# Optimization experiments

Hardware: AMD Instinct MI355X
Metric: run time of the kernel (lower is better)

## Reference

```python
import jax, jax.numpy as jnp
import numpy as np

N, E, B = 100000, 3200000, 1024
D_LM, K, H, C, L = 1024, 128, 256, 40, 2
T = 0.1
LN_EPS = 1e-5


def _layernorm(x, g, b):
    m = x.mean(-1, keepdims=True)
    v = ((x - m) ** 2).mean(-1, keepdims=True)
    return (x - m) * jax.lax.rsqrt(v + LN_EPS) * g + b


def _gcn_conv(x, W, b, src, dst, norm, self_w):
    h = x @ W
    agg = jax.ops.segment_sum(h[src] * norm[:, None], dst, num_segments=N)
    return agg + h * self_w[:, None] + b


def setup_inputs() -> dict:
    key = jax.random.key(0)
    ks = jax.random.split(key, 20)
    s = 0.02
    rn = lambda k, shp: jax.random.normal(k, shp, jnp.float32) * s
    return {
        "hidden_embeds": jax.random.normal(ks[0], (L, N, D_LM), jnp.float32),
        "proj_W1": rn(ks[1], (L, D_LM, K)),
        "proj_b1": jnp.zeros((L, K), jnp.float32),
        "ln_g": jnp.ones((L, K), jnp.float32),
        "ln_b": jnp.zeros((L, K), jnp.float32),
        "proj_W2": rn(ks[2], (L, K, K)),
        "proj_b2": jnp.zeros((L, K), jnp.float32),
        "alphas": jnp.zeros((L,), jnp.float32),
        "gcn_W1": rn(ks[3], (L, K, H)),
        "gcn_b1": jnp.zeros((L, H), jnp.float32),
        "gcn_W2": rn(ks[4], (L, H, K)),
        "gcn_b2": jnp.zeros((L, K), jnp.float32),
        "clf_W": rn(ks[5], (2 * K, C)),
        "clf_b": jnp.zeros((C,), jnp.float32),
        "edge_index": jax.random.randint(ks[6], (2, E), 0, N, jnp.int64 if jax.config.jax_enable_x64 else jnp.int32),
        "mapping": jax.random.randint(ks[7], (B,), 0, N, jnp.int64 if jax.config.jax_enable_x64 else jnp.int32),
    }


def reference(hidden_embeds, proj_W1, proj_b1, ln_g, ln_b, proj_W2, proj_b2,
              alphas, gcn_W1, gcn_b1, gcn_W2, gcn_b2, clf_W, clf_b,
              edge_index, mapping):
    src, dst = edge_index[0], edge_index[1]
    ones = jnp.ones((E,), jnp.float32)
    # GCN normalization (self loops included): deg over dst + 1
    deg = jax.ops.segment_sum(ones, dst, num_segments=N) + 1.0
    dis = jax.lax.rsqrt(deg)
    norm = dis[src] * dis[dst]          # per-edge D^-1/2 A D^-1/2
    self_w = 1.0 / deg                  # self-loop weight dis[i]*dis[i]

    last = None
    for i in range(L):
        # projector: Linear -> LayerNorm -> ReLU -> Linear
        h = hidden_embeds[i] @ proj_W1[i] + proj_b1[i]
        h = jax.nn.relu(_layernorm(h, ln_g[i], ln_b[i]))
        h = h @ proj_W2[i] + proj_b2[i]
        if i > 0:
            a = jax.nn.sigmoid(alphas[i] / T)
            h = h * a + last * (1.0 - a)
        # 2-layer GCN encoder (dropout=0)
        z = jax.nn.relu(_gcn_conv(h, gcn_W1[i], gcn_b1[i], src, dst, norm, self_w))
        last = _gcn_conv(z, gcn_W2[i], gcn_b2[i], src, dst, norm, self_w)

    # custom_global_mean_pool: mean over {node} U {out-neighbors} U {in-neighbors}
    sum_n = (jax.ops.segment_sum(last[dst], src, num_segments=N)
             + jax.ops.segment_sum(last[src], dst, num_segments=N))
    cnt = (jax.ops.segment_sum(ones, src, num_segments=N)
           + jax.ops.segment_sum(ones, dst, num_segments=N))
    pooled = (last[mapping] + sum_n[mapping]) / (1.0 + cnt[mapping])[:, None]

    out = jnp.concatenate([last[mapping], pooled], axis=1)  # [B, 2K]
    return out @ clf_W + clf_b
```

## Files before the change

### kernel.cpp

```cpp
#include <hip/hip_runtime.h>
#include <hip/hip_bf16.h>
#include <math.h>

using short8 = __attribute__((ext_vector_type(8))) short;
using f32x4  = __attribute__((ext_vector_type(4))) float;

#define PSTRIDE 2048

__device__ __forceinline__ short f2bf(float f) {
    __hip_bfloat16 h = __float2bfloat16(f);
    return *reinterpret_cast<short*>(&h);
}


__global__ void map_scatter_k(const int* __restrict__ mapping, int* __restrict__ map_idx, int B)
{
    int b = blockIdx.x * blockDim.x + threadIdx.x;
    if (b < B) map_idx[mapping[b]] = b;
}

__launch_bounds__(1024)
__global__ void bin_count_k(const int* __restrict__ dst, int E, int* __restrict__ bin_cnt)
{
    __shared__ int h[4096];
    for (int i = threadIdx.x; i < 4096; i += 1024) h[i] = 0;
    __syncthreads();
    int base = blockIdx.x * 32768;
#pragma unroll
    for (int i = 0; i < 32; ++i) {
        int e = base + i * 1024 + threadIdx.x;
        if (e < E) atomicAdd(&h[dst[e] >> 5], 1);
    }
    __syncthreads();
    for (int i = threadIdx.x; i < 4096; i += 1024) {
        int c = h[i];
        if (c) atomicAdd(&bin_cnt[i], c);
    }
}

__launch_bounds__(1024)
__global__ void scan_bins_k(const int* __restrict__ cnt, int* __restrict__ off,
                            int* __restrict__ cur)
{
    __shared__ int wsum[16];
    int tid = threadIdx.x, lane = tid & 63, wid = tid >> 6;
    int4 v = ((const int4*)cnt)[tid];
    int s0 = v.x, s1 = s0 + v.y, s2 = s1 + v.z, s3 = s2 + v.w;
    int q = s3;
#pragma unroll
    for (int o = 1; o < 64; o <<= 1) { int t = __shfl_up(q, o); if (lane >= o) q += t; }
    if (lane == 63) wsum[wid] = q;
    __syncthreads();
    if (wid == 0) {
        int w = (lane < 16) ? wsum[lane] : 0;
#pragma unroll
        for (int o = 1; o < 16; o <<= 1) { int t = __shfl_up(w, o); if (lane >= o) w += t; }
        if (lane < 16) wsum[lane] = w;
    }
    __syncthreads();
    int base = (wid ? wsum[wid - 1] : 0) + q - s3;
    int4 o4; o4.x = base; o4.y = base + s0; o4.z = base + s1; o4.w = base + s2;
    ((int4*)off)[tid] = o4;
    ((int4*)cur)[tid] = o4;
    if (tid == 1023) off[4096] = base + s3;
}

__launch_bounds__(256)
__global__ void bin_scatter_k(const int* __restrict__ ei, int E,
                              const int* __restrict__ map_idx,
                              int* __restrict__ bin_cur, int2* __restrict__ pairs,
                              int* __restrict__ pcnt, int* __restrict__ pnb)
{
    int e = blockIdx.x * blockDim.x + threadIdx.x;
    if (e >= E) return;
    int s = ei[e];
    int d = ei[E + e];
    int p = atomicAdd(&bin_cur[d >> 5], 1);
    pairs[p] = make_int2(s, d);
    int ms = map_idx[s];
    if (ms >= 0) {
        int i = atomicAdd(&pcnt[ms], 1);
        if (i < PSTRIDE) pnb[ms * PSTRIDE + i] = d;
    }
    int md = map_idx[d];
    if (md >= 0) {
        int i = atomicAdd(&pcnt[md], 1);
        if (i < PSTRIDE) pnb[md * PSTRIDE + i] = s;
    }
}

__launch_bounds__(256)
__global__ void bin_csr_k(const int2* __restrict__ pairs, const int* __restrict__ bin_off,
                          int* __restrict__ csr_in, int* __restrict__ in_off,
                          float* __restrict__ dis, float* __restrict__ selfw, int N)
{
    __shared__ int lcnt[32];
    __shared__ int lofs[32];
    __shared__ int lcur[32];
    int b = blockIdx.x;
    int tid = threadIdx.x;
    if (tid < 32) lcnt[tid] = 0;
    __syncthreads();
    int beg = bin_off[b], end = bin_off[b + 1];
    for (int i = beg + tid; i < end; i += 256)
        atomicAdd(&lcnt[pairs[i].y & 31], 1);
    __syncthreads();
    if (tid == 0) {
        int run = beg;
#pragma unroll
        for (int j = 0; j < 32; ++j) { lofs[j] = run; lcur[j] = run; run += lcnt[j]; }
    }
    __syncthreads();
    int n0 = b * 32;
    if (tid < 32 && n0 + tid < N) {
        in_off[n0 + tid] = lofs[tid];
        float dg = (float)lcnt[tid] + 1.0f;
        dis[n0 + tid] = rsqrtf(dg);
        selfw[n0 + tid] = 1.0f / dg;
    }
    if (b == gridDim.x - 1 && tid == 0) in_off[N] = end;
    for (int i = beg + tid; i < end; i += 256) {
        int2 pr = pairs[i];
        int p = atomicAdd(&lcur[pr.y & 31], 1);
        csr_in[p] = pr.x;
    }
}

__global__ void transpose_w_k(const float* __restrict__ src, short* __restrict__ dst,
                              int R, int Cc)
{
    int idx = blockIdx.x * blockDim.x + threadIdx.x;
    if (idx >= R * Cc) return;
    int r = idx / Cc;
    int c = idx - r * Cc;
    dst[(size_t)c * R + r] = f2bf(src[idx]);
}

__launch_bounds__(256)
__global__ void proj_fused_k(const float* __restrict__ X,
                             const short* __restrict__ W1t,
                             const float* __restrict__ b1,
                             const float* __restrict__ lng,
                             const float* __restrict__ lnb,
                             const short* __restrict__ W2t,
                             const float* __restrict__ b2,
                             const float* __restrict__ alphas, int layer,
                             const float* __restrict__ last,
                             short* __restrict__ out, int nrows)
{
    __shared__ short S[26112];

    const int tid  = threadIdx.x;
    const int lane = tid & 63;
    const int wave = tid >> 6;
    const int g    = lane >> 4;
    const int lr   = lane & 15;
    const int wrow = wave * 16;
    const int row0 = blockIdx.x * 64;

    f32x4 acc[8];
#pragma unroll
    for (int f = 0; f < 8; ++f) acc[f] = (f32x4){0.f, 0.f, 0.f, 0.f};

    for (int k0 = 0; k0 < 1024; k0 += 64) {
        {
            int r  = tid >> 2;
            int c0 = (tid & 3) * 16;
            int gr = row0 + r;
            float4 v0 = make_float4(0.f,0.f,0.f,0.f), v1 = v0, v2 = v0, v3 = v0;
            if (gr < nrows) {
                const float* xp = X + (size_t)gr * 1024 + k0 + c0;
                v0 = *(const float4*)&xp[0];
                v1 = *(const float4*)&xp[4];
                v2 = *(const float4*)&xp[8];
                v3 = *(const float4*)&xp[12];
            }
            short8 p0, p1;
            p0[0]=f2bf(v0.x); p0[1]=f2bf(v0.y); p0[2]=f2bf(v0.z); p0[3]=f2bf(v0.w);
            p0[4]=f2bf(v1.x); p0[5]=f2bf(v1.y); p0[6]=f2bf(v1.z); p0[7]=f2bf(v1.w);
            p1[0]=f2bf(v2.x); p1[1]=f2bf(v2.y); p1[2]=f2bf(v2.z); p1[3]=f2bf(v2.w);
            p1[4]=f2bf(v3.x); p1[5]=f2bf(v3.y); p1[6]=f2bf(v3.z); p1[7]=f2bf(v3.w);
            *(short8*)&S[r * 72 + c0]     = p0;
            *(short8*)&S[r * 72 + c0 + 8] = p1;
        }
        {
            int c  = tid >> 1;
            int kb = (tid & 1) * 32;
            const short* wp = W1t + (size_t)c * 1024 + k0 + kb;
            short* dp = &S[4608 + c * 72 + kb];
#pragma unroll
            for (int m = 0; m < 4; ++m)
                *(short8*)&dp[m * 8] = *(const short8*)&wp[m * 8];
        }
        __syncthreads();
#pragma unroll
        for (int kk = 0; kk < 64; kk += 32) {
            short8 a = *(short8*)&S[(wrow + lr) * 72 + kk + g * 8];
#pragma unroll
            for (int f = 0; f < 8; ++f) {
                short8 b = *(short8*)&S[4608 + (f * 16 + lr) * 72 + kk + g * 8];
                acc[f] = __builtin_amdgcn_mfma_f32_16x16x32_bf16(a, b, acc[f], 0, 0, 0);
            }
        }
        __syncthreads();
    }

    {
        float b1v[8], gv[8], bv[8];
#pragma unroll
        for (int f = 0; f < 8; ++f) {
            int col = f * 16 + lr;
            b1v[f] = b1[col]; gv[f] = lng[col]; bv[f] = lnb[col];
        }
#pragma unroll
        for (int j = 0; j < 4; ++j) {
            float hv[8];
            float s = 0.f, q = 0.f;
#pragma unroll
            for (int f = 0; f < 8; ++f) {
                float t = acc[f][j] + b1v[f];
                hv[f] = t;
                s += t; q += t * t;
            }
#pragma unroll
            for (int m = 1; m < 16; m <<= 1) {
                s += __shfl_xor(s, m);
                q += __shfl_xor(q, m);
            }
            float mean = s * (1.0f / 128.0f);
            float var  = q * (1.0f / 128.0f) - mean * mean;
            float inv  = rsqrtf(var + 1e-5f);
            int rloc = wrow + 4 * g + j;
#pragma unroll
            for (int f = 0; f < 8; ++f) {
                float h = fmaxf((hv[f] - mean) * inv * gv[f] + bv[f], 0.f);
                S[17408 + rloc * 136 + f * 16 + lr] = f2bf(h);
            }
        }
    }
    {
        int c  = tid >> 1;
        int kb = (tid & 1) * 64;
        const short* wp = W2t + (size_t)c * 128 + kb;
        short* dp = &S[c * 136 + kb];
#pragma unroll
        for (int m = 0; m < 8; ++m)
            *(short8*)&dp[m * 8] = *(const short8*)&wp[m * 8];
    }
    __syncthreads();

    f32x4 acc2[8];
#pragma unroll
    for (int f = 0; f < 8; ++f) acc2[f] = (f32x4){0.f, 0.f, 0.f, 0.f};
#pragma unroll
    for (int kk = 0; kk < 128; kk += 32) {
        short8 a = *(short8*)&S[17408 + (wrow + lr) * 136 + kk + g * 8];
#pragma unroll
        for (int f = 0; f < 8; ++f) {
            short8 b = *(short8*)&S[(f * 16 + lr) * 136 + kk + g * 8];
            acc2[f] = __builtin_amdgcn_mfma_f32_16x16x32_bf16(a, b, acc2[f], 0, 0, 0);
        }
    }

    float b2v[8];
#pragma unroll
    for (int f = 0; f < 8; ++f) b2v[f] = b2[f * 16 + lr];
    float asig = 0.f, omas = 0.f;
    if (last) {
        float al = alphas[layer];
        asig = 1.0f / (1.0f + expf(-al * 10.0f));
        omas = 1.0f - asig;
    }
#pragma unroll
    for (int j = 0; j < 4; ++j) {
        int gr = row0 + wrow + 4 * g + j;
        if (gr >= nrows) continue;
#pragma unroll
        for (int f = 0; f < 8; ++f) {
            int col = f * 16 + lr;
            float o = acc2[f][j] + b2v[f];
            if (last) o = asig * o + omas * last[(size_t)gr * 128 + col];
            out[(size_t)gr * 128 + col] = f2bf(o);
        }
    }
}

__launch_bounds__(256)
__global__ void gcn_mlp_k(const short* __restrict__ U,
                          const short* __restrict__ W1t,
                          const float* __restrict__ gb1,
                          const short* __restrict__ W2t,
                          short* __restrict__ V, int M)
{
    __shared__ short S[35840];

    const int tid  = threadIdx.x;
    const int lane = tid & 63;
    const int wave = tid >> 6;
    const int g    = lane >> 4;
    const int lr   = lane & 15;
    const int wrow = wave * 16;
    const int m0   = blockIdx.x * 64;

#pragma unroll
    for (int it = 0; it < 4; ++it) {
        int i = tid + it * 256;
        int r = i >> 4;
        int c8 = i & 15;
        short8 v = {0,0,0,0,0,0,0,0};
        int gr = m0 + r;
        if (gr < M) v = *(const short8*)&U[(size_t)gr * 128 + c8 * 8];
        *(short8*)&S[r * 136 + c8 * 8] = v;
    }

    f32x4 acc[16];
#pragma unroll
    for (int f = 0; f < 16; ++f) acc[f] = (f32x4){0.f, 0.f, 0.f, 0.f};

    for (int k0 = 0; k0 < 128; k0 += 64) {
#pragma unroll
        for (int it = 0; it < 8; ++it) {
            int i = tid + it * 256;
            int r = i >> 3;
            int c8 = i & 7;
            *(short8*)&S[17408 + r * 72 + c8 * 8] =
                *(const short8*)&W1t[(size_t)r * 128 + k0 + c8 * 8];
        }
        __syncthreads();
#pragma unroll
        for (int kk = 0; kk < 64; kk += 32) {
            short8 a = *(short8*)&S[(wrow + lr) * 136 + k0 + kk + g * 8];
#pragma unroll
            for (int f = 0; f < 16; ++f) {
                short8 b = *(short8*)&S[17408 + (f * 16 + lr) * 72 + kk + g * 8];
                acc[f] = __builtin_amdgcn_mfma_f32_16x16x32_bf16(a, b, acc[f], 0, 0, 0);
            }
        }
        __syncthreads();
    }

    {
        float bb[16];
#pragma unroll
        for (int f = 0; f < 16; ++f) bb[f] = gb1[f * 16 + lr];
#pragma unroll
        for (int j = 0; j < 4; ++j) {
            int rloc = wrow + 4 * g + j;
#pragma unroll
            for (int f = 0; f < 16; ++f) {
                float zv = fmaxf(acc[f][j] + bb[f], 0.f);
                S[rloc * 264 + f * 16 + lr] = f2bf(zv);
            }
        }
    }

    f32x4 acc2[8];
#pragma unroll
    for (int f = 0; f < 8; ++f) acc2[f] = (f32x4){0.f, 0.f, 0.f, 0.f};

    for (int k0 = 0; k0 < 256; k0 += 64) {
#pragma unroll
        for (int it = 0; it < 4; ++it) {
            int i = tid + it * 256;
            int r = i >> 3;
            int c8 = i & 7;
            *(short8*)&S[16896 + r * 72 + c8 * 8] =
                *(const short8*)&W2t[(size_t)r * 256 + k0 + c8 * 8];
        }
        __syncthreads();
#pragma unroll
        for (int kk = 0; kk < 64; kk += 32) {
            short8 a = *(short8*)&S[(wrow + lr) * 264 + k0 + kk + g * 8];
#pragma unroll
            for (int f = 0; f < 8; ++f) {
                short8 b = *(short8*)&S[16896 + (f * 16 + lr) * 72 + kk + g * 8];
                acc2[f] = __builtin_amdgcn_mfma_f32_16x16x32_bf16(a, b, acc2[f], 0, 0, 0);
            }
        }
        __syncthreads();
    }

#pragma unroll
    for (int j = 0; j < 4; ++j) {
        int gr = m0 + wrow + 4 * g + j;
        if (gr >= M) continue;
#pragma unroll
        for (int f = 0; f < 8; ++f)
            V[(size_t)gr * 128 + f * 16 + lr] = f2bf(acc2[f][j]);
    }
}

template <bool OUT_BF16>
__launch_bounds__(256)
__global__ void agg_k(const unsigned* __restrict__ x, void* __restrict__ y,
                      const int* __restrict__ off, const int* __restrict__ csr,
                      const float* __restrict__ dis, const float* __restrict__ selfw,
                      const float* __restrict__ bias, int N)
{
    int node = blockIdx.x * 4 + (threadIdx.x >> 6);
    if (node >= N) return;
    int lane = threadIdx.x & 63;
    int beg = off[node], end = off[node + 1];

    float ax0 = 0.f, ay0 = 0.f, ax1 = 0.f, ay1 = 0.f;
    float ax2 = 0.f, ay2 = 0.f, ax3 = 0.f, ay3 = 0.f;
    int e = beg;
    for (; e + 4 <= end; e += 4) {
        int s0 = csr[e], s1 = csr[e + 1], s2 = csr[e + 2], s3 = csr[e + 3];
        unsigned v0 = x[(size_t)s0 * 64 + lane];
        unsigned v1 = x[(size_t)s1 * 64 + lane];
        unsigned v2 = x[(size_t)s2 * 64 + lane];
        unsigned v3 = x[(size_t)s3 * 64 + lane];
        float w0 = dis[s0], w1 = dis[s1], w2 = dis[s2], w3 = dis[s3];
        ax0 = fmaf(w0, __uint_as_float(v0 << 16), ax0);
        ay0 = fmaf(w0, __uint_as_float(v0 & 0xFFFF0000u), ay0);
        ax1 = fmaf(w1, __uint_as_float(v1 << 16), ax1);
        ay1 = fmaf(w1, __uint_as_float(v1 & 0xFFFF0000u), ay1);
        ax2 = fmaf(w2, __uint_as_float(v2 << 16), ax2);
        ay2 = fmaf(w2, __uint_as_float(v2 & 0xFFFF0000u), ay2);
        ax3 = fmaf(w3, __uint_as_float(v3 << 16), ax3);
        ay3 = fmaf(w3, __uint_as_float(v3 & 0xFFFF0000u), ay3);
    }
    for (; e < end; ++e) {
        int s = csr[e];
        float w = dis[s];
        unsigned v = x[(size_t)s * 64 + lane];
        ax0 = fmaf(w, __uint_as_float(v << 16), ax0);
        ay0 = fmaf(w, __uint_as_float(v & 0xFFFF0000u), ay0);
    }
    float accx = (ax0 + ax1) + (ax2 + ax3);
    float accy = (ay0 + ay1) + (ay2 + ay3);

    float dn = dis[node], sw = selfw[node];
    unsigned vo = x[(size_t)node * 64 + lane];
    float rx = dn * accx + sw * __uint_as_float(vo << 16);
    float ry = dn * accy + sw * __uint_as_float(vo & 0xFFFF0000u);
    if (bias) { rx += bias[lane * 2]; ry += bias[lane * 2 + 1]; }
    if (OUT_BF16) {
        unsigned p = (unsigned)(unsigned short)f2bf(rx) | ((unsigned)(unsigned short)f2bf(ry) << 16);
        ((unsigned*)y)[(size_t)node * 64 + lane] = p;
    } else {
        *(float2*)&((float*)y)[(size_t)node * 128 + lane * 2] = make_float2(rx, ry);
    }
}

__launch_bounds__(128)
__global__ void pool_clf_k(const float* __restrict__ last, const int* __restrict__ mapping,
                           const int* __restrict__ map_idx,
                           const int* __restrict__ pcnt, const int* __restrict__ pnb,
                           const float* __restrict__ clfW, const float* __restrict__ clfb,
                           float* __restrict__ out, int C)
{
    int b = blockIdx.x;
    int tid = threadIdx.x;
    int n = mapping[b];
    int rep = map_idx[n];
    int cnt = pcnt[rep];
    int m = cnt < PSTRIDE ? cnt : PSTRIDE;

    float s = 0.f;
    const int* nb = pnb + (size_t)rep * PSTRIDE;
    for (int i = 0; i < m; ++i)
        s += last[(size_t)nb[i] * 128 + tid];

    float lv = last[(size_t)n * 128 + tid];
    float pooled = (lv + s) / (1.0f + (float)cnt);

    __shared__ float feat[256];
    feat[tid] = lv;
    feat[128 + tid] = pooled;
    __syncthreads();

    for (int c = tid; c < C; c += blockDim.x) {
        float o = clfb[c];
        for (int j = 0; j < 256; ++j) o = fmaf(feat[j], clfW[j * C + c], o);
        out[(size_t)b * C + c] = o;
    }
}

extern "C" void kernel_launch(void* const* d_in, const int* in_sizes, int n_in,
                              void* d_out, int out_size, void* d_ws, size_t ws_size,
                              hipStream_t stream)
{
    const float* hidden = (const float*)d_in[0];
    const float* pW1    = (const float*)d_in[1];
    const float* pb1    = (const float*)d_in[2];
    const float* lng    = (const float*)d_in[3];
    const float* lnb    = (const float*)d_in[4];
    const float* pW2    = (const float*)d_in[5];
    const float* pb2    = (const float*)d_in[6];
    const float* alphas = (const float*)d_in[7];
    const float* gW1    = (const float*)d_in[8];
    const float* gb1    = (const float*)d_in[9];
    const float* gW2    = (const float*)d_in[10];
    const float* gb2    = (const float*)d_in[11];
    const float* clfW   = (const float*)d_in[12];
    const float* clfb   = (const float*)d_in[13];
    const int*   ei     = (const int*)d_in[14];
    const int*   mapping= (const int*)d_in[15];

    const int L   = in_sizes[7];
    const int K   = in_sizes[2] / L;
    const int H   = in_sizes[9] / L;
    const int C   = in_sizes[13];
    const int DLM = in_sizes[1] / (L * K);
    const int N   = in_sizes[0] / (L * DLM);
    const int E   = in_sizes[14] / 2;
    const int B   = in_sizes[15];
    const int NBINS = (N + 31) / 32;

    char* ws = (char*)d_ws;
    size_t off = 0;
    auto carve = [&](size_t bytes) -> char* {
        char* p = ws + off;
        off += (bytes + 255) & ~(size_t)255;
        return p;
    };
    int*   map_idx = (int*)carve((size_t)N * 4);
    int*   pcnt    = (int*)carve((size_t)B * 4);
    int*   pnb     = (int*)carve((size_t)B * PSTRIDE * 4);
    int*   bin_cnt = (int*)carve(4096 * 4);
    int*   bin_off = (int*)carve(4097 * 4);
    int*   bin_cur = (int*)carve(4096 * 4);
    int2*  pairs   = (int2*)carve((size_t)E * 8);
    int*   in_off  = (int*)carve((size_t)(N + 1) * 4);
    float* dis     = (float*)carve((size_t)N * 4);
    float* selfw   = (float*)carve((size_t)N * 4);
    int*   csr_in  = (int*)carve((size_t)E * 4);
    short* bufA    = (short*)carve((size_t)N * K * 2);
    short* bufU    = (short*)carve((size_t)N * K * 2);
    float* bufLast = (float*)carve((size_t)N * K * 4);
    short* w1t     = (short*)carve((size_t)L * K * DLM * 2);
    short* w2t     = (short*)carve((size_t)L * K * K * 2);
    short* gw1t    = (short*)carve((size_t)L * H * K * 2);
    short* gw2t    = (short*)carve((size_t)L * K * H * 2);
    (void)ws_size; (void)n_in; (void)out_size;

    hipMemsetAsync(bin_cnt, 0, 4096 * 4, stream);
    hipMemsetAsync(map_idx, 0xFF, (size_t)N * 4, stream);
    hipMemsetAsync(pcnt, 0, (size_t)B * 4, stream);
    map_scatter_k<<<dim3((B + 255) / 256), 256, 0, stream>>>(mapping, map_idx, B);
    bin_count_k<<<dim3((E + 32767) / 32768), 1024, 0, stream>>>(ei + E, E, bin_cnt);
    scan_bins_k<<<dim3(1), 1024, 0, stream>>>(bin_cnt, bin_off, bin_cur);
    bin_scatter_k<<<dim3((E + 255) / 256), 256, 0, stream>>>(ei, E, map_idx, bin_cur,
                                                             pairs, pcnt, pnb);
    bin_csr_k<<<dim3(NBINS), 256, 0, stream>>>(pairs, bin_off, csr_in, in_off,
                                               dis, selfw, N);

    for (int i = 0; i < L; ++i) {
        transpose_w_k<<<dim3((DLM * K + 255) / 256), 256, 0, stream>>>(
            pW1 + (size_t)i * DLM * K, w1t + (size_t)i * K * DLM, DLM, K);
        transpose_w_k<<<dim3((K * K + 255) / 256), 256, 0, stream>>>(
            pW2 + (size_t)i * K * K, w2t + (size_t)i * K * K, K, K);
        transpose_w_k<<<dim3((K * H + 255) / 256), 256, 0, stream>>>(
            gW1 + (size_t)i * K * H, gw1t + (size_t)i * H * K, K, H);
        transpose_w_k<<<dim3((H * K + 255) / 256), 256, 0, stream>>>(
            gW2 + (size_t)i * H * K, gw2t + (size_t)i * K * H, H, K);
    }

    const int nblk64 = (N + 63) / 64;

    for (int i = 0; i < L; ++i) {
        proj_fused_k<<<dim3(nblk64), 256, 0, stream>>>(
            hidden + (size_t)i * N * DLM,
            w1t + (size_t)i * K * DLM,
            pb1 + (size_t)i * K,
            lng + (size_t)i * K,
            lnb + (size_t)i * K,
            w2t + (size_t)i * K * K,
            pb2 + (size_t)i * K,
            alphas, i,
            (i > 0) ? bufLast : nullptr,
            bufA, N);

        agg_k<true><<<dim3((N + 3) / 4), 256, 0, stream>>>(
            (const unsigned*)bufA, bufU, in_off, csr_in, dis, selfw, nullptr, N);
        gcn_mlp_k<<<dim3(nblk64), 256, 0, stream>>>(
            bufU, gw1t + (size_t)i * H * K, gb1 + (size_t)i * H,
            gw2t + (size_t)i * K * H, bufA, N);
        agg_k<false><<<dim3((N + 3) / 4), 256, 0, stream>>>(
            (const unsigned*)bufA, bufLast, in_off, csr_in, dis, selfw,
            gb2 + (size_t)i * K, N);
    }

    pool_clf_k<<<dim3(B), 128, 0, stream>>>(bufLast, mapping, map_idx, pcnt, pnb,
                                            clfW, clfb, (float*)d_out, C);
}
```

Measured before the change: 1.285 ms.

## Double projector tile to 128 rows with 512 threads; unroll edge gather to 8

The fused projector kernel now processes 128 rows per block with 8 waves, so each W1 and W2 tile staged in shared memory is reused by twice as many rows. The W2 stage is reorganised into two 64-wide K chunks so it fits the new LDS layout. Separately, the aggregation kernel unrolls its neighbor gather from 4 to 8 independent loads to raise memory-level parallelism. The costs are fewer blocks in flight and more registers per thread in the aggregation loop.

```diff
diff --git a/kernel.cpp b/kernel.cpp
--- a/kernel.cpp
+++ b/kernel.cpp
@@ -136,7 +136,7 @@
     dst[(size_t)c * R + r] = f2bf(src[idx]);
 }
 
-__launch_bounds__(256)
+__launch_bounds__(512)
 __global__ void proj_fused_k(const float* __restrict__ X,
                              const short* __restrict__ W1t,
                              const float* __restrict__ b1,
@@ -148,7 +148,7 @@
                              const float* __restrict__ last,
                              short* __restrict__ out, int nrows)
 {
-    __shared__ short S[26112];
+    __shared__ short S[26624];
 
     const int tid  = threadIdx.x;
     const int lane = tid & 63;
@@ -156,7 +156,7 @@
     const int g    = lane >> 4;
     const int lr   = lane & 15;
     const int wrow = wave * 16;
-    const int row0 = blockIdx.x * 64;
+    const int row0 = blockIdx.x * 128;
 
     f32x4 acc[8];
 #pragma unroll
@@ -184,13 +184,11 @@
             *(short8*)&S[r * 72 + c0 + 8] = p1;
         }
         {
-            int c  = tid >> 1;
-            int kb = (tid & 1) * 32;
+            int c  = tid >> 2;
+            int kb = (tid & 3) * 16;
             const short* wp = W1t + (size_t)c * 1024 + k0 + kb;
-            short* dp = &S[4608 + c * 72 + kb];
-#pragma unroll
-            for (int m = 0; m < 4; ++m)
-                *(short8*)&dp[m * 8] = *(const short8*)&wp[m * 8];
+            *(short8*)&S[9216 + c * 72 + kb]     = *(const short8*)&wp[0];
+            *(short8*)&S[9216 + c * 72 + kb + 8] = *(const short8*)&wp[8];
         }
         __syncthreads();
 #pragma unroll
@@ -198,7 +196,7 @@
             short8 a = *(short8*)&S[(wrow + lr) * 72 + kk + g * 8];
 #pragma unroll
             for (int f = 0; f < 8; ++f) {
-                short8 b = *(short8*)&S[4608 + (f * 16 + lr) * 72 + kk + g * 8];
+                short8 b = *(short8*)&S[9216 + (f * 16 + lr) * 72 + kk + g * 8];
                 acc[f] = __builtin_amdgcn_mfma_f32_16x16x32_bf16(a, b, acc[f], 0, 0, 0);
             }
         }
@@ -234,32 +232,33 @@
 #pragma unroll
             for (int f = 0; f < 8; ++f) {
                 float h = fmaxf((hv[f] - mean) * inv * gv[f] + bv[f], 0.f);
-                S[17408 + rloc * 136 + f * 16 + lr] = f2bf(h);
-            }
-        }
-    }
-    {
-        int c  = tid >> 1;
-        int kb = (tid & 1) * 64;
-        const short* wp = W2t + (size_t)c * 128 + kb;
-        short* dp = &S[c * 136 + kb];
-#pragma unroll
-        for (int m = 0; m < 8; ++m)
-            *(short8*)&dp[m * 8] = *(const short8*)&wp[m * 8];
-    }
-    __syncthreads();
+                S[rloc * 136 + f * 16 + lr] = f2bf(h);
+            }
+        }
+    }
 
     f32x4 acc2[8];
 #pragma unroll
     for (int f = 0; f < 8; ++f) acc2[f] = (f32x4){0.f, 0.f, 0.f, 0.f};
-#pragma unroll
-    for (int kk = 0; kk < 128; kk += 32) {
-        short8 a = *(short8*)&S[17408 + (wrow + lr) * 136 + kk + g * 8];
-#pragma unroll
-        for (int f = 0; f < 8; ++f) {
-            short8 b = *(short8*)&S[(f * 16 + lr) * 136 + kk + g * 8];
-            acc2[f] = __builtin_amdgcn_mfma_f32_16x16x32_bf16(a, b, acc2[f], 0, 0, 0);
-        }
+    for (int k0 = 0; k0 < 128; k0 += 64) {
+        {
+            int c  = tid >> 2;
+            int kb = (tid & 3) * 16;
+            const short* wp = W2t + (size_t)c * 128 + k0 + kb;
+            *(short8*)&S[17408 + c * 72 + kb]     = *(const short8*)&wp[0];
+            *(short8*)&S[17408 + c * 72 + kb + 8] = *(const short8*)&wp[8];
+        }
+        __syncthreads();
+#pragma unroll
+        for (int kk = 0; kk < 64; kk += 32) {
+            short8 a = *(short8*)&S[(wrow + lr) * 136 + k0 + kk + g * 8];
+#pragma unroll
+            for (int f = 0; f < 8; ++f) {
+                short8 b = *(short8*)&S[17408 + (f * 16 + lr) * 72 + kk + g * 8];
+                acc2[f] = __builtin_amdgcn_mfma_f32_16x16x32_bf16(a, b, acc2[f], 0, 0, 0);
+            }
+        }
+        __syncthreads();
     }
 
     float b2v[8];
@@ -402,34 +401,36 @@
     int lane = threadIdx.x & 63;
     int beg = off[node], end = off[node + 1];
 
-    float ax0 = 0.f, ay0 = 0.f, ax1 = 0.f, ay1 = 0.f;
-    float ax2 = 0.f, ay2 = 0.f, ax3 = 0.f, ay3 = 0.f;
+    float ax[8], ay[8];
+#pragma unroll
+    for (int u = 0; u < 8; ++u) { ax[u] = 0.f; ay[u] = 0.f; }
+
     int e = beg;
-    for (; e + 4 <= end; e += 4) {
-        int s0 = csr[e], s1 = csr[e + 1], s2 = csr[e + 2], s3 = csr[e + 3];
-        unsigned v0 = x[(size_t)s0 * 64 + lane];
-        unsigned v1 = x[(size_t)s1 * 64 + lane];
-        unsigned v2 = x[(size_t)s2 * 64 + lane];
-        unsigned v3 = x[(size_t)s3 * 64 + lane];
-        float w0 = dis[s0], w1 = dis[s1], w2 = dis[s2], w3 = dis[s3];
-        ax0 = fmaf(w0, __uint_as_float(v0 << 16), ax0);
-        ay0 = fmaf(w0, __uint_as_float(v0 & 0xFFFF0000u), ay0);
-        ax1 = fmaf(w1, __uint_as_float(v1 << 16), ax1);
-        ay1 = fmaf(w1, __uint_as_float(v1 & 0xFFFF0000u), ay1);
-        ax2 = fmaf(w2, __uint_as_float(v2 << 16), ax2);
-        ay2 = fmaf(w2, __uint_as_float(v2 & 0xFFFF0000u), ay2);
-        ax3 = fmaf(w3, __uint_as_float(v3 << 16), ax3);
-        ay3 = fmaf(w3, __uint_as_float(v3 & 0xFFFF0000u), ay3);
+    for (; e + 8 <= end; e += 8) {
+        int   ss[8];
+        unsigned vv[8];
+        float ww[8];
+#pragma unroll
+        for (int u = 0; u < 8; ++u) ss[u] = csr[e + u];
+#pragma unroll
+        for (int u = 0; u < 8; ++u) vv[u] = x[(size_t)ss[u] * 64 + lane];
+#pragma unroll
+        for (int u = 0; u < 8; ++u) ww[u] = dis[ss[u]];
+#pragma unroll
+        for (int u = 0; u < 8; ++u) {
+            ax[u] = fmaf(ww[u], __uint_as_float(vv[u] << 16), ax[u]);
+            ay[u] = fmaf(ww[u], __uint_as_float(vv[u] & 0xFFFF0000u), ay[u]);
+        }
     }
     for (; e < end; ++e) {
         int s = csr[e];
         float w = dis[s];
         unsigned v = x[(size_t)s * 64 + lane];
-        ax0 = fmaf(w, __uint_as_float(v << 16), ax0);
-        ay0 = fmaf(w, __uint_as_float(v & 0xFFFF0000u), ay0);
-    }
-    float accx = (ax0 + ax1) + (ax2 + ax3);
-    float accy = (ay0 + ay1) + (ay2 + ay3);
+        ax[0] = fmaf(w, __uint_as_float(v << 16), ax[0]);
+        ay[0] = fmaf(w, __uint_as_float(v & 0xFFFF0000u), ay[0]);
+    }
+    float accx = ((ax[0] + ax[1]) + (ax[2] + ax[3])) + ((ax[4] + ax[5]) + (ax[6] + ax[7]));
+    float accy = ((ay[0] + ay[1]) + (ay[2] + ay[3])) + ((ay[4] + ay[5]) + (ay[6] + ay[7]));
 
     float dn = dis[node], sw = selfw[node];
     unsigned vo = x[(size_t)node * 64 + lane];
@@ -558,10 +559,11 @@
             gW2 + (size_t)i * H * K, gw2t + (size_t)i * K * H, H, K);
     }
 
-    const int nblk64 = (N + 63) / 64;
+    const int nblk64  = (N + 63) / 64;
+    const int nblk128 = (N + 127) / 128;
 
     for (int i = 0; i < L; ++i) {
-        proj_fused_k<<<dim3(nblk64), 256, 0, stream>>>(
+        proj_fused_k<<<dim3(nblk128), 512, 0, stream>>>(
             hidden + (size_t)i * N * DLM,
             w1t + (size_t)i * K * DLM,
             pb1 + (size_t)i * K,
```

New measurement: 1.322 ms. 2.9% more time.

## Use 2D warp tiling with 128-row blocks in projector and GCN MLP GEMMs

Applied to the files above, without the earlier changes.

The projector kernel now processes 128 rows per block with a 2x2 wave grid, each wave computing a 64x64 output tile. Because each wave now holds only half the columns, the LayerNorm row statistics are reduced across waves through shared memory. The GCN MLP kernel switches from row-split waves to column-split waves, each covering all 64 rows. The aim is to reuse each loaded A and B fragment across several MFMAs and cut LDS read traffic per MFMA, at the cost of more accumulator registers and an extra barrier.

```diff
diff --git a/kernel.cpp b/kernel.cpp
--- a/kernel.cpp
+++ b/kernel.cpp
@@ -148,123 +148,162 @@
                              const float* __restrict__ last,
                              short* __restrict__ out, int nrows)
 {
-    __shared__ short S[26112];
+    __shared__ short S[26624];
 
     const int tid  = threadIdx.x;
     const int lane = tid & 63;
     const int wave = tid >> 6;
+    const int wr   = wave >> 1;
+    const int wc   = wave & 1;
     const int g    = lane >> 4;
     const int lr   = lane & 15;
-    const int wrow = wave * 16;
-    const int row0 = blockIdx.x * 64;
-
-    f32x4 acc[8];
-#pragma unroll
-    for (int f = 0; f < 8; ++f) acc[f] = (f32x4){0.f, 0.f, 0.f, 0.f};
+    const int row0 = blockIdx.x * 128;
+
+    f32x4 acc[4][4];
+#pragma unroll
+    for (int fr = 0; fr < 4; ++fr)
+#pragma unroll
+        for (int fc = 0; fc < 4; ++fc) acc[fr][fc] = (f32x4){0.f, 0.f, 0.f, 0.f};
 
     for (int k0 = 0; k0 < 1024; k0 += 64) {
         {
-            int r  = tid >> 2;
-            int c0 = (tid & 3) * 16;
-            int gr = row0 + r;
-            float4 v0 = make_float4(0.f,0.f,0.f,0.f), v1 = v0, v2 = v0, v3 = v0;
+            int r    = tid >> 1;
+            int c0   = (tid & 1) * 32;
+            int gr   = row0 + r;
+            float4 v[8];
             if (gr < nrows) {
                 const float* xp = X + (size_t)gr * 1024 + k0 + c0;
-                v0 = *(const float4*)&xp[0];
-                v1 = *(const float4*)&xp[4];
-                v2 = *(const float4*)&xp[8];
-                v3 = *(const float4*)&xp[12];
+#pragma unroll
+                for (int m = 0; m < 8; ++m) v[m] = *(const float4*)&xp[m * 4];
+            } else {
+#pragma unroll
+                for (int m = 0; m < 8; ++m) v[m] = make_float4(0.f, 0.f, 0.f, 0.f);
             }
-            short8 p0, p1;
-            p0[0]=f2bf(v0.x); p0[1]=f2bf(v0.y); p0[2]=f2bf(v0.z); p0[3]=f2bf(v0.w);
-            p0[4]=f2bf(v1.x); p0[5]=f2bf(v1.y); p0[6]=f2bf(v1.z); p0[7]=f2bf(v1.w);
-            p1[0]=f2bf(v2.x); p1[1]=f2bf(v2.y); p1[2]=f2bf(v2.z); p1[3]=f2bf(v2.w);
-            p1[4]=f2bf(v3.x); p1[5]=f2bf(v3.y); p1[6]=f2bf(v3.z); p1[7]=f2bf(v3.w);
-            *(short8*)&S[r * 72 + c0]     = p0;
-            *(short8*)&S[r * 72 + c0 + 8] = p1;
+#pragma unroll
+            for (int m = 0; m < 4; ++m) {
+                short8 p;
+                p[0]=f2bf(v[2*m].x); p[1]=f2bf(v[2*m].y); p[2]=f2bf(v[2*m].z); p[3]=f2bf(v[2*m].w);
+                p[4]=f2bf(v[2*m+1].x); p[5]=f2bf(v[2*m+1].y); p[6]=f2bf(v[2*m+1].z); p[7]=f2bf(v[2*m+1].w);
+                *(short8*)&S[r * 72 + c0 + m * 8] = p;
+            }
         }
         {
             int c  = tid >> 1;
             int kb = (tid & 1) * 32;
             const short* wp = W1t + (size_t)c * 1024 + k0 + kb;
-            short* dp = &S[4608 + c * 72 + kb];
 #pragma unroll
             for (int m = 0; m < 4; ++m)
-                *(short8*)&dp[m * 8] = *(const short8*)&wp[m * 8];
+                *(short8*)&S[9216 + c * 72 + kb + m * 8] = *(const short8*)&wp[m * 8];
         }
         __syncthreads();
 #pragma unroll
         for (int kk = 0; kk < 64; kk += 32) {
-            short8 a = *(short8*)&S[(wrow + lr) * 72 + kk + g * 8];
-#pragma unroll
-            for (int f = 0; f < 8; ++f) {
-                short8 b = *(short8*)&S[4608 + (f * 16 + lr) * 72 + kk + g * 8];
-                acc[f] = __builtin_amdgcn_mfma_f32_16x16x32_bf16(a, b, acc[f], 0, 0, 0);
+            short8 a[4], b[4];
+#pragma unroll
+            for (int fr = 0; fr < 4; ++fr)
+                a[fr] = *(short8*)&S[(wr * 64 + fr * 16 + lr) * 72 + kk + g * 8];
+#pragma unroll
+            for (int fc = 0; fc < 4; ++fc)
+                b[fc] = *(short8*)&S[9216 + (wc * 64 + fc * 16 + lr) * 72 + kk + g * 8];
+#pragma unroll
+            for (int fr = 0; fr < 4; ++fr)
+#pragma unroll
+                for (int fc = 0; fc < 4; ++fc)
+                    acc[fr][fc] = __builtin_amdgcn_mfma_f32_16x16x32_bf16(a[fr], b[fc], acc[fr][fc], 0, 0, 0);
+        }
+        __syncthreads();
+    }
+
+    float* P = (float*)&S[17408];
+    {
+        float b1v[4], gv[4], bv[4];
+#pragma unroll
+        for (int fc = 0; fc < 4; ++fc) {
+            int col = wc * 64 + fc * 16 + lr;
+            b1v[fc] = b1[col]; gv[fc] = lng[col]; bv[fc] = lnb[col];
+        }
+        float hv[4][4];
+#pragma unroll
+        for (int fr = 0; fr < 4; ++fr) {
+#pragma unroll
+            for (int j = 0; j < 4; ++j) {
+                float s = 0.f, q = 0.f;
+#pragma unroll
+                for (int fc = 0; fc < 4; ++fc) {
+                    float t = acc[fr][fc][j] + b1v[fc];
+                    acc[fr][fc][j] = t;
+                    s += t; q += t * t;
+                }
+#pragma unroll
+                for (int m = 1; m < 16; m <<= 1) {
+                    s += __shfl_xor(s, m);
+                    q += __shfl_xor(q, m);
+                }
+                if (lr == 0) {
+                    int row = wr * 64 + fr * 16 + 4 * g + j;
+                    P[row * 4 + wc * 2]     = s;
+                    P[row * 4 + wc * 2 + 1] = q;
+                }
             }
         }
         __syncthreads();
-    }
-
-    {
-        float b1v[8], gv[8], bv[8];
-#pragma unroll
-        for (int f = 0; f < 8; ++f) {
-            int col = f * 16 + lr;
-            b1v[f] = b1[col]; gv[f] = lng[col]; bv[f] = lnb[col];
-        }
-#pragma unroll
-        for (int j = 0; j < 4; ++j) {
-            float hv[8];
-            float s = 0.f, q = 0.f;
-#pragma unroll
-            for (int f = 0; f < 8; ++f) {
-                float t = acc[f][j] + b1v[f];
-                hv[f] = t;
-                s += t; q += t * t;
+#pragma unroll
+        for (int fr = 0; fr < 4; ++fr) {
+#pragma unroll
+            for (int j = 0; j < 4; ++j) {
+                int row = wr * 64 + fr * 16 + 4 * g + j;
+                float s = P[row * 4 + 0] + P[row * 4 + 2];
+                float q = P[row * 4 + 1] + P[row * 4 + 3];
+                float mean = s * (1.0f / 128.0f);
+                float var  = q * (1.0f / 128.0f) - mean * mean;
+                float inv  = rsqrtf(var + 1e-5f);
+#pragma unroll
+                for (int fc = 0; fc < 4; ++fc) {
+                    float h = fmaxf((acc[fr][fc][j] - mean) * inv * gv[fc] + bv[fc], 0.f);
+                    S[row * 136 + wc * 64 + fc * 16 + lr] = f2bf(h);
+                }
             }
-#pragma unroll
-            for (int m = 1; m < 16; m <<= 1) {
-                s += __shfl_xor(s, m);
-                q += __shfl_xor(q, m);
-            }
-            float mean = s * (1.0f / 128.0f);
-            float var  = q * (1.0f / 128.0f) - mean * mean;
-            float inv  = rsqrtf(var + 1e-5f);
-            int rloc = wrow + 4 * g + j;
-#pragma unroll
-            for (int f = 0; f < 8; ++f) {
-                float h = fmaxf((hv[f] - mean) * inv * gv[f] + bv[f], 0.f);
-                S[17408 + rloc * 136 + f * 16 + lr] = f2bf(h);
-            }
-        }
-    }
-    {
-        int c  = tid >> 1;
-        int kb = (tid & 1) * 64;
-        const short* wp = W2t + (size_t)c * 128 + kb;
-        short* dp = &S[c * 136 + kb];
-#pragma unroll
-        for (int m = 0; m < 8; ++m)
-            *(short8*)&dp[m * 8] = *(const short8*)&wp[m * 8];
-    }
-    __syncthreads();
-
-    f32x4 acc2[8];
-#pragma unroll
-    for (int f = 0; f < 8; ++f) acc2[f] = (f32x4){0.f, 0.f, 0.f, 0.f};
-#pragma unroll
-    for (int kk = 0; kk < 128; kk += 32) {
-        short8 a = *(short8*)&S[17408 + (wrow + lr) * 136 + kk + g * 8];
-#pragma unroll
-        for (int f = 0; f < 8; ++f) {
-            short8 b = *(short8*)&S[(f * 16 + lr) * 136 + kk + g * 8];
-            acc2[f] = __builtin_amdgcn_mfma_f32_16x16x32_bf16(a, b, acc2[f], 0, 0, 0);
-        }
-    }
-
-    float b2v[8];
-#pragma unroll
-    for (int f = 0; f < 8; ++f) b2v[f] = b2[f * 16 + lr];
+        }
+    }
+    __syncthreads();
+
+    f32x4 acc2[4][4];
+#pragma unroll
+    for (int fr = 0; fr < 4; ++fr)
+#pragma unroll
+        for (int fc = 0; fc < 4; ++fc) acc2[fr][fc] = (f32x4){0.f, 0.f, 0.f, 0.f};
+
+    for (int k0 = 0; k0 < 128; k0 += 64) {
+        {
+            int c  = tid >> 1;
+            int kb = (tid & 1) * 32;
+            const short* wp = W2t + (size_t)c * 128 + k0 + kb;
+#pragma unroll
+            for (int m = 0; m < 4; ++m)
+                *(short8*)&S[17408 + c * 72 + kb + m * 8] = *(const short8*)&wp[m * 8];
+        }
+        __syncthreads();
+#pragma unroll
+        for (int kk = 0; kk < 64; kk += 32) {
+            short8 a[4], b[4];
+#pragma unroll
+            for (int fr = 0; fr < 4; ++fr)
+                a[fr] = *(short8*)&S[(wr * 64 + fr * 16 + lr) * 136 + k0 + kk + g * 8];
+#pragma unroll
+            for (int fc = 0; fc < 4; ++fc)
+                b[fc] = *(short8*)&S[17408 + (wc * 64 + fc * 16 + lr) * 72 + kk + g * 8];
+#pragma unroll
+            for (int fr = 0; fr < 4; ++fr)
+#pragma unroll
+                for (int fc = 0; fc < 4; ++fc)
+                    acc2[fr][fc] = __builtin_amdgcn_mfma_f32_16x16x32_bf16(a[fr], b[fc], acc2[fr][fc], 0, 0, 0);
+        }
+        __syncthreads();
+    }
+
+    float b2v[4];
+#pragma unroll
+    for (int fc = 0; fc < 4; ++fc) b2v[fc] = b2[wc * 64 + fc * 16 + lr];
     float asig = 0.f, omas = 0.f;
     if (last) {
         float al = alphas[layer];
@@ -272,15 +311,18 @@
         omas = 1.0f - asig;
     }
 #pragma unroll
-    for (int j = 0; j < 4; ++j) {
-        int gr = row0 + wrow + 4 * g + j;
-        if (gr >= nrows) continue;
-#pragma unroll
-        for (int f = 0; f < 8; ++f) {
-            int col = f * 16 + lr;
-            float o = acc2[f][j] + b2v[f];
-            if (last) o = asig * o + omas * last[(size_t)gr * 128 + col];
-            out[(size_t)gr * 128 + col] = f2bf(o);
+    for (int fr = 0; fr < 4; ++fr) {
+#pragma unroll
+        for (int j = 0; j < 4; ++j) {
+            int gr = row0 + wr * 64 + fr * 16 + 4 * g + j;
+            if (gr >= nrows) continue;
+#pragma unroll
+            for (int fc = 0; fc < 4; ++fc) {
+                int col = wc * 64 + fc * 16 + lr;
+                float o = acc2[fr][fc][j] + b2v[fc];
+                if (last) o = asig * o + omas * last[(size_t)gr * 128 + col];
+                out[(size_t)gr * 128 + col] = f2bf(o);
+            }
         }
     }
 }
@@ -299,7 +341,6 @@
     const int wave = tid >> 6;
     const int g    = lane >> 4;
     const int lr   = lane & 15;
-    const int wrow = wave * 16;
     const int m0   = blockIdx.x * 64;
 
 #pragma unroll
@@ -313,9 +354,11 @@
         *(short8*)&S[r * 136 + c8 * 8] = v;
     }
 
-    f32x4 acc[16];
-#pragma unroll
-    for (int f = 0; f < 16; ++f) acc[f] = (f32x4){0.f, 0.f, 0.f, 0.f};
+    f32x4 acc[4][4];
+#pragma unroll
+    for (int fr = 0; fr < 4; ++fr)
+#pragma unroll
+        for (int fc = 0; fc < 4; ++fc) acc[fr][fc] = (f32x4){0.f, 0.f, 0.f, 0.f};
 
     for (int k0 = 0; k0 < 128; k0 += 64) {
 #pragma unroll
@@ -329,34 +372,46 @@
         __syncthreads();
 #pragma unroll
         for (int kk = 0; kk < 64; kk += 32) {
-            short8 a = *(short8*)&S[(wrow + lr) * 136 + k0 + kk + g * 8];
-#pragma unroll
-            for (int f = 0; f < 16; ++f) {
-                short8 b = *(short8*)&S[17408 + (f * 16 + lr) * 72 + kk + g * 8];
-                acc[f] = __builtin_amdgcn_mfma_f32_16x16x32_bf16(a, b, acc[f], 0, 0, 0);
+            short8 a[4], b[4];
+#pragma unroll
+            for (int fr = 0; fr < 4; ++fr)
+                a[fr] = *(short8*)&S[(fr * 16 + lr) * 136 + k0 + kk + g * 8];
+#pragma unroll
+            for (int fc = 0; fc < 4; ++fc)
+                b[fc] = *(short8*)&S[17408 + (wave * 64 + fc * 16 + lr) * 72 + kk + g * 8];
+#pragma unroll
+            for (int fr = 0; fr < 4; ++fr)
+#pragma unroll
+                for (int fc = 0; fc < 4; ++fc)
+                    acc[fr][fc] = __builtin_amdgcn_mfma_f32_16x16x32_bf16(a[fr], b[fc], acc[fr][fc], 0, 0, 0);
+        }
+        __syncthreads();
+    }
+
+    {
+        float bb[4];
+#pragma unroll
+        for (int fc = 0; fc < 4; ++fc) bb[fc] = gb1[wave * 64 + fc * 16 + lr];
+#pragma unroll
+        for (int fr = 0; fr < 4; ++fr) {
+#pragma unroll
+            for (int j = 0; j < 4; ++j) {
+                int rloc = fr * 16 + 4 * g + j;
+#pragma unroll
+                for (int fc = 0; fc < 4; ++fc) {
+                    float zv = fmaxf(acc[fr][fc][j] + bb[fc], 0.f);
+                    S[rloc * 264 + wave * 64 + fc * 16 + lr] = f2bf(zv);
+                }
             }
         }
-        __syncthreads();
-    }
-
-    {
-        float bb[16];
-#pragma unroll
-        for (int f = 0; f < 16; ++f) bb[f] = gb1[f * 16 + lr];
-#pragma unroll
-        for (int j = 0; j < 4; ++j) {
-            int rloc = wrow + 4 * g + j;
-#pragma unroll
-            for (int f = 0; f < 16; ++f) {
-                float zv = fmaxf(acc[f][j] + bb[f], 0.f);
-                S[rloc * 264 + f * 16 + lr] = f2bf(zv);
-            }
-        }
-    }
-
-    f32x4 acc2[8];
-#pragma unroll
-    for (int f = 0; f < 8; ++f) acc2[f] = (f32x4){0.f, 0.f, 0.f, 0.f};
+    }
+
+    f32x4 acc2[4][2];
+#pragma unroll
+    for (int fr = 0; fr < 4; ++fr) {
+        acc2[fr][0] = (f32x4){0.f, 0.f, 0.f, 0.f};
+        acc2[fr][1] = (f32x4){0.f, 0.f, 0.f, 0.f};
+    }
 
     for (int k0 = 0; k0 < 256; k0 += 64) {
 #pragma unroll
@@ -370,23 +425,32 @@
         __syncthreads();
 #pragma unroll
         for (int kk = 0; kk < 64; kk += 32) {
-            short8 a = *(short8*)&S[(wrow + lr) * 264 + k0 + kk + g * 8];
-#pragma unroll
-            for (int f = 0; f < 8; ++f) {
-                short8 b = *(short8*)&S[16896 + (f * 16 + lr) * 72 + kk + g * 8];
-                acc2[f] = __builtin_amdgcn_mfma_f32_16x16x32_bf16(a, b, acc2[f], 0, 0, 0);
-            }
-        }
-        __syncthreads();
-    }
-
-#pragma unroll
-    for (int j = 0; j < 4; ++j) {
-        int gr = m0 + wrow + 4 * g + j;
-        if (gr >= M) continue;
-#pragma unroll
-        for (int f = 0; f < 8; ++f)
-            V[(size_t)gr * 128 + f * 16 + lr] = f2bf(acc2[f][j]);
+            short8 a[4], b[2];
+#pragma unroll
+            for (int fr = 0; fr < 4; ++fr)
+                a[fr] = *(short8*)&S[(fr * 16 + lr) * 264 + k0 + kk + g * 8];
+#pragma unroll
+            for (int fc = 0; fc < 2; ++fc)
+                b[fc] = *(short8*)&S[16896 + (wave * 32 + fc * 16 + lr) * 72 + kk + g * 8];
+#pragma unroll
+            for (int fr = 0; fr < 4; ++fr)
+#pragma unroll
+                for (int fc = 0; fc < 2; ++fc)
+                    acc2[fr][fc] = __builtin_amdgcn_mfma_f32_16x16x32_bf16(a[fr], b[fc], acc2[fr][fc], 0, 0, 0);
+        }
+        __syncthreads();
+    }
+
+#pragma unroll
+    for (int fr = 0; fr < 4; ++fr) {
+#pragma unroll
+        for (int j = 0; j < 4; ++j) {
+            int gr = m0 + fr * 16 + 4 * g + j;
+            if (gr >= M) continue;
+#pragma unroll
+            for (int fc = 0; fc < 2; ++fc)
+                V[(size_t)gr * 128 + wave * 32 + fc * 16 + lr] = f2bf(acc2[fr][fc][j]);
+        }
     }
 }
 
@@ -558,10 +622,11 @@
             gW2 + (size_t)i * H * K, gw2t + (size_t)i * K * H, H, K);
     }
 
-    const int nblk64 = (N + 63) / 64;
+    const int nblk64  = (N + 63) / 64;
+    const int nblk128 = (N + 127) / 128;
 
     for (int i = 0; i < L; ++i) {
-        proj_fused_k<<<dim3(nblk64), 256, 0, stream>>>(
+        proj_fused_k<<<dim3(nblk128), 256, 0, stream>>>(
             hidden + (size_t)i * N * DLM,
             w1t + (size_t)i * K * DLM,
             pb1 + (size_t)i * K,
```

Result: slower. 1.311 ms (+2.1%).
